# Optimization experiments

Measured on AMD Instinct MI355X. Metric: run time of the kernel, lower is better.

Reference implementation:

```python
import jax, jax.numpy as jnp
import numpy as np


def setup_inputs() -> dict:
    key = jax.random.key(0)
    k1, k2, k3, k4 = jax.random.split(key, 4)
    B, C, H, W = 4, 64, 128, 256
    Cout, kH, kW = 64, 3, 3
    x = jax.random.normal(k1, (B, C, H, W), dtype=jnp.float32)
    # offset layout: channel 2*(i*kW+j) = dy, 2*(i*kW+j)+1 = dx (deformable_groups=1)
    offset = jax.random.normal(k2, (B, 2 * kH * kW, H, W), dtype=jnp.float32)
    weight = jax.random.normal(k3, (Cout, C, kH, kW), dtype=jnp.float32) * 0.05
    bias = jax.random.normal(k4, (Cout,), dtype=jnp.float32) * 0.05
    return {"x": x, "offset": offset, "weight": weight, "bias": bias}


STRIDE, PAD, DIL = 1, 1, 1


def _deform_conv(x, offset, weight, bias):
    B, C, H, W = x.shape
    Cout, Cin, kH, kW = weight.shape
    K = kH * kW
    Ho = (H + 2 * PAD - DIL * (kH - 1) - 1) // STRIDE + 1
    Wo = (W + 2 * PAD - DIL * (kW - 1) - 1) // STRIDE + 1

    hs = (jnp.arange(Ho) * STRIDE - PAD).astype(jnp.float32)  # [Ho]
    ws = (jnp.arange(Wo) * STRIDE - PAD).astype(jnp.float32)  # [Wo]
    ki, kj = jnp.meshgrid(jnp.arange(kH), jnp.arange(kW), indexing="ij")
    ki = (ki.reshape(K) * DIL).astype(jnp.float32)  # [K]
    kj = (kj.reshape(K) * DIL).astype(jnp.float32)

    off = offset.reshape(B, K, 2, Ho, Wo)
    dy, dx = off[:, :, 0], off[:, :, 1]  # [B,K,Ho,Wo]
    py = hs[None, None, :, None] + ki[None, :, None, None] + dy  # [B,K,Ho,Wo]
    px = ws[None, None, None, :] + kj[None, :, None, None] + dx

    y0 = jnp.floor(py)
    x0 = jnp.floor(px)
    ly = py - y0
    lx = px - x0
    y0i = y0.astype(jnp.int32)
    x0i = x0.astype(jnp.int32)

    def gather(xb, yi, xi):
        # xb: [C,H,W]; yi, xi: [K,Ho,Wo]; zero for out-of-bounds corners
        valid = (yi >= 0) & (yi < H) & (xi >= 0) & (xi < W)
        yc = jnp.clip(yi, 0, H - 1)
        xc = jnp.clip(xi, 0, W - 1)
        idx = (yc * W + xc).reshape(-1)
        g = jnp.take(xb.reshape(C, H * W), idx, axis=1).reshape(C, K, Ho, Wo)
        return g * valid[None].astype(xb.dtype)

    gather_b = jax.vmap(gather)
    corners = [
        (y0i, x0i, (1.0 - ly) * (1.0 - lx)),
        (y0i, x0i + 1, (1.0 - ly) * lx),
        (y0i + 1, x0i, ly * (1.0 - lx)),
        (y0i + 1, x0i + 1, ly * lx),
    ]
    vals = jnp.zeros((B, C, K, Ho, Wo), dtype=x.dtype)
    for yi, xi, w in corners:
        vals = vals + gather_b(x, yi, xi) * w[:, None]  # broadcast over C

    out = jnp.einsum("bckhw,ock->bohw", vals, weight.reshape(Cout, Cin, K))
    return out + bias[None, :, None, None]


def reference(x, offset, weight, bias):
    return _deform_conv(x, offset, weight, bias)
```

## Files before the change

kernel.cpp:

```cpp
#include <hip/hip_runtime.h>

typedef float floatx4 __attribute__((ext_vector_type(4)));
typedef _Float16 half2v __attribute__((ext_vector_type(2)));
typedef _Float16 half8 __attribute__((ext_vector_type(8)));

#define Hh 128
#define Ww 256
#define Cc 64
#define COUT 64
#define Bb 4
#define HW (Hh*Ww)
#define VP 74

__global__ void prep(const float* __restrict__ x, const float* __restrict__ wsrc,
                     _Float16* __restrict__ xn, unsigned short* __restrict__ wdst) {
    const int bx = blockIdx.x, h = blockIdx.y, b = blockIdx.z;
    const int tid = threadIdx.x;
    if (bx == 2) {
        const int i = (h + Hh * b) * 72 + tid;
        if (tid < 72) {
            const int kt = i % 9, c = (i / 9) % Cc, o = i / (9 * Cc);
            _Float16 hv = (_Float16)wsrc[i];
            wdst[(kt * COUT + o) * Cc + c] = *(unsigned short*)&hv;
        }
        return;
    }
    __shared__ unsigned short T[128][VP];
    const int wl = tid & 127;
    const int ch = tid >> 7;
    const float* sp = x + ((b * Cc + ch * 32) * Hh + h) * Ww + bx * 128 + wl;
#pragma unroll
    for (int c2 = 0; c2 < 16; ++c2) {
        const float v0 = sp[(2 * c2) * HW];
        const float v1 = sp[(2 * c2 + 1) * HW];
        half2v hv; hv.x = (_Float16)v0; hv.y = (_Float16)v1;
        *(unsigned*)&T[wl][ch * 32 + 2 * c2] = *(unsigned*)&hv;
    }
    __syncthreads();
    uint4* drow = (uint4*)(xn + ((size_t)(b * Hh + h) * Ww + bx * 128) * 64);
#pragma unroll
    for (int j = 0; j < 4; ++j) {
        const int idx = j * 256 + tid;
        drow[idx] = *(const uint4*)&T[idx >> 3][(idx & 7) * 8];
    }
}

__device__ __forceinline__ void lds_barrier() {
    asm volatile("s_waitcnt lgkmcnt(0)\n\ts_barrier" ::: "memory");
}

struct Tap {
    half2v W00, W01, W10, W11;
    int a00, a01, a10, a11;
};

__device__ __forceinline__ void tap_setup(int kt, int h, int w, float dy, float dx,
                                          int cg, Tap& t) {
    const int ki = kt / 3, kj = kt % 3;
    const float py = (float)(h - 1 + ki) + dy;
    const float px = (float)(w - 1 + kj) + dx;
    const float y0f = floorf(py), x0f = floorf(px);
    const int y0 = (int)y0f, x0 = (int)x0f;
    const float ly = py - y0f, lx = px - x0f;
    const int y1 = y0 + 1, x1 = x0 + 1;
    const bool vy0 = ((unsigned)y0 < Hh), vy1 = ((unsigned)y1 < Hh);
    const bool vx0 = ((unsigned)x0 < Ww), vx1 = ((unsigned)x1 < Ww);
    const float w00 = (vy0 && vx0) ? (1.f - ly) * (1.f - lx) : 0.f;
    const float w01 = (vy0 && vx1) ? (1.f - ly) * lx : 0.f;
    const float w10 = (vy1 && vx0) ? ly * (1.f - lx) : 0.f;
    const float w11 = (vy1 && vx1) ? ly * lx : 0.f;
    _Float16 h00 = (_Float16)w00, h01 = (_Float16)w01;
    _Float16 h10 = (_Float16)w10, h11 = (_Float16)w11;
    t.W00.x = h00; t.W00.y = h00;  t.W01.x = h01; t.W01.y = h01;
    t.W10.x = h10; t.W10.y = h10;  t.W11.x = h11; t.W11.y = h11;
    const int y0c = min(max(y0, 0), Hh - 1), y1c = min(max(y1, 0), Hh - 1);
    const int x0c = min(max(x0, 0), Ww - 1), x1c = min(max(x1, 0), Ww - 1);
    t.a00 = (y0c * Ww + x0c) * 8 + cg;
    t.a01 = (y0c * Ww + x1c) * 8 + cg;
    t.a10 = (y1c * Ww + x0c) * 8 + cg;
    t.a11 = (y1c * Ww + x1c) * 8 + cg;
}

__device__ __forceinline__ void tap_load(const uint4* __restrict__ xb4, const Tap& t,
                                         unsigned (&pf)[16]) {
    *(uint4*)&pf[0]  = xb4[t.a00];
    *(uint4*)&pf[4]  = xb4[t.a01];
    *(uint4*)&pf[8]  = xb4[t.a10];
    *(uint4*)&pf[12] = xb4[t.a11];
}

__device__ __forceinline__ void wf_load(const unsigned short* __restrict__ wt,
                                        half8 (&WF)[4]) {
    WF[0] = *(const half8*)(wt);
    WF[1] = *(const half8*)(wt + 16 * Cc);
    WF[2] = *(const half8*)(wt + 32);
    WF[3] = *(const half8*)(wt + 16 * Cc + 32);
}

__device__ __forceinline__ void tap_store(const Tap& t, const unsigned (&pf)[16],
                                          unsigned short* __restrict__ vrow) {
    unsigned o[4];
#pragma unroll
    for (int s = 0; s < 4; ++s) {
        half2v v = (*(const half2v*)&pf[s])      * t.W00
                 + (*(const half2v*)&pf[4 + s])  * t.W01
                 + (*(const half2v*)&pf[8 + s])  * t.W10
                 + (*(const half2v*)&pf[12 + s]) * t.W11;
        o[s] = *(unsigned*)&v;
    }
    uint4 u; u.x = o[0]; u.y = o[1]; u.z = o[2]; u.w = o[3];
    *(uint4*)vrow = u;
}

__device__ __forceinline__ void mfma_tap(const half8 (&WF)[4],
                                         const unsigned short* __restrict__ Vbuf,
                                         int nt, int ln, floatx4 (&acc)[2]) {
#pragma unroll
    for (int g = 0; g < 2; ++g) {
        const int pp = nt * 16 + (ln & 15);
        half8 bfrag = *(const half8*)&Vbuf[pp * VP + g * 32 + (ln >> 4) * 8];
        acc[0] = __builtin_amdgcn_mfma_f32_16x16x32_f16(WF[2 * g],     bfrag, acc[0], 0, 0, 0);
        acc[1] = __builtin_amdgcn_mfma_f32_16x16x32_f16(WF[2 * g + 1], bfrag, acc[1], 0, 0, 0);
    }
}

template<int KT>
__device__ __forceinline__ void pipe_iter(
    const uint4* __restrict__ xb4, const float* __restrict__ offb,
    const unsigned short* __restrict__ wfb,
    const unsigned short* __restrict__ V0, const unsigned short* __restrict__ V1,
    unsigned short* __restrict__ vrow0, unsigned short* __restrict__ vrow1,
    int h, int w, int cg, int nt, int ln,
    Tap& tp0, Tap& tp1, unsigned (&pf0)[16], unsigned (&pf1)[16],
    half8 (&WF0)[4], half8 (&WF1)[4],
    float& dy0, float& dx0, float& dy1, float& dx1,
    floatx4 (&acc)[2])
{
    constexpr int S = KT & 1, T = 1 - S;
    wf_load(wfb + KT * COUT * Cc, S ? WF1 : WF0);
    if constexpr (KT < 8) {
        tap_setup(KT + 1, h, w, T ? dy1 : dy0, T ? dx1 : dx0, cg, T ? tp1 : tp0);
        tap_load(xb4, T ? tp1 : tp0, T ? pf1 : pf0);
    }
    if constexpr (KT + 3 <= 8) {
        (T ? dy1 : dy0) = offb[(2 * (KT + 3)) * HW];
        (T ? dx1 : dx0) = offb[(2 * (KT + 3) + 1) * HW];
    }
    mfma_tap(T ? WF1 : WF0, T ? V1 : V0, nt, ln, acc);
    tap_store(S ? tp1 : tp0, S ? pf1 : pf0, S ? vrow1 : vrow0);
    lds_barrier();
}

__launch_bounds__(256, 4)
__global__ void dcn_mfma(const _Float16* __restrict__ xn,
                         const float* __restrict__ offset,
                         const unsigned short* __restrict__ wb,
                         const float* __restrict__ bias,
                         float* __restrict__ out) {
    __shared__ unsigned short V[2][32 * VP];

    const int tid = threadIdx.x;
    const int p   = tid >> 3;
    const int cg  = tid & 7;
    const int wv  = tid >> 6;
    const int ln  = tid & 63;

    const int b  = blockIdx.z;
    const int h  = blockIdx.y;
    const int w0 = blockIdx.x * 32;
    const int w  = w0 + p;

    const uint4* xb4  = (const uint4*)(xn + (size_t)b * HW * 64);
    const float* offb = offset + b * 18 * HW + h * Ww + w;
    unsigned short* vrow0 = &V[0][p * VP + cg * 8];
    unsigned short* vrow1 = &V[1][p * VP + cg * 8];

    const int nt = wv & 1;
    const int mb = (wv >> 1) * 2;
    const unsigned short* wfb = wb + (mb * 16 + (ln & 15)) * Cc + (ln >> 4) * 8;

    floatx4 acc[2];
    acc[0] = (floatx4)0.f; acc[1] = (floatx4)0.f;

    unsigned pf0[16], pf1[16];
    half8 WF0[4], WF1[4];
    Tap tp0, tp1;

    float dy0 = offb[0],        dx0 = offb[HW];
    float dy1 = offb[2 * HW],   dx1 = offb[3 * HW];
    wf_load(wfb, WF0);
    tap_setup(0, h, w, dy0, dx0, cg, tp0);
    tap_load(xb4, tp0, pf0);
    tap_setup(1, h, w, dy1, dx1, cg, tp1);
    tap_load(xb4, tp1, pf1);
    dy0 = offb[4 * HW]; dx0 = offb[5 * HW];
    dy1 = offb[6 * HW]; dx1 = offb[7 * HW];
    tap_store(tp0, pf0, vrow0);
    lds_barrier();

#define PI(K) pipe_iter<K>(xb4, offb, wfb, V[0], V[1], vrow0, vrow1, h, w, cg, nt, ln, \
                           tp0, tp1, pf0, pf1, WF0, WF1, dy0, dx0, dy1, dx1, acc)
    PI(1); PI(2); PI(3); PI(4); PI(5); PI(6); PI(7); PI(8);
#undef PI

    mfma_tap(WF0, V[0], nt, ln, acc);

    float* outp = out + b * COUT * HW + h * Ww;
    const int col = w0 + nt * 16 + (ln & 15);
#pragma unroll
    for (int mi = 0; mi < 2; ++mi)
#pragma unroll
        for (int r = 0; r < 4; ++r) {
            const int o = (mb + mi) * 16 + (ln >> 4) * 4 + r;
            outp[o * HW + col] = acc[mi][r] + bias[o];
        }
}

extern "C" void kernel_launch(void* const* d_in, const int* in_sizes, int n_in,
                              void* d_out, int out_size, void* d_ws, size_t ws_size,
                              hipStream_t stream) {
    const float* x      = (const float*)d_in[0];
    const float* offset = (const float*)d_in[1];
    const float* weight = (const float*)d_in[2];
    const float* bias   = (const float*)d_in[3];
    float* out = (float*)d_out;

    _Float16* xn = (_Float16*)d_ws;
    unsigned short* wb = (unsigned short*)((char*)d_ws + (size_t)Bb * HW * Cc * 2);

    prep<<<dim3(3, Hh, Bb), 256, 0, stream>>>(x, weight, xn, wb);
    dcn_mfma<<<dim3(Ww / 32, Hh, Bb), 256, 0, stream>>>(xn, offset, wb, bias, out);
}
```

Baseline: 176.3 us.

## Build MFMA B-fragments in registers directly, dropping LDS staging and barriers

Each wave now gathers and bilinearly combines the sampled pixels straight into its own MFMA B-operand registers, so every lane covers one output column and one 8-channel group. The shared-memory V buffer and the per-tap barriers are removed. Each wave computes all 64 output channels for 16 columns (4 accumulators), and each block covers 64 columns instead of 32. In exchange, every wave has to load all weight fragments itself, and the gather loads are split into two half-channel stages per tap, which raises register pressure.

```diff
diff --git a/kernel.cpp b/kernel.cpp
--- a/kernel.cpp
+++ b/kernel.cpp
@@ -45,17 +45,13 @@
     }
 }
 
-__device__ __forceinline__ void lds_barrier() {
-    asm volatile("s_waitcnt lgkmcnt(0)\n\ts_barrier" ::: "memory");
-}
-
-struct Tap {
+struct TapS {
     half2v W00, W01, W10, W11;
     int a00, a01, a10, a11;
 };
 
 __device__ __forceinline__ void tap_setup(int kt, int h, int w, float dy, float dx,
-                                          int cg, Tap& t) {
+                                          int kg, TapS& t) {
     const int ki = kt / 3, kj = kt % 3;
     const float py = (float)(h - 1 + ki) + dy;
     const float px = (float)(w - 1 + kj) + dx;
@@ -75,80 +71,62 @@
     t.W10.x = h10; t.W10.y = h10;  t.W11.x = h11; t.W11.y = h11;
     const int y0c = min(max(y0, 0), Hh - 1), y1c = min(max(y1, 0), Hh - 1);
     const int x0c = min(max(x0, 0), Ww - 1), x1c = min(max(x1, 0), Ww - 1);
-    t.a00 = (y0c * Ww + x0c) * 8 + cg;
-    t.a01 = (y0c * Ww + x1c) * 8 + cg;
-    t.a10 = (y1c * Ww + x0c) * 8 + cg;
-    t.a11 = (y1c * Ww + x1c) * 8 + cg;
+    t.a00 = (y0c * Ww + x0c) * 8 + kg;
+    t.a01 = (y0c * Ww + x1c) * 8 + kg;
+    t.a10 = (y1c * Ww + x0c) * 8 + kg;
+    t.a11 = (y1c * Ww + x1c) * 8 + kg;
 }
 
-__device__ __forceinline__ void tap_load(const uint4* __restrict__ xb4, const Tap& t,
-                                         unsigned (&pf)[16]) {
-    *(uint4*)&pf[0]  = xb4[t.a00];
-    *(uint4*)&pf[4]  = xb4[t.a01];
-    *(uint4*)&pf[8]  = xb4[t.a10];
-    *(uint4*)&pf[12] = xb4[t.a11];
+__device__ __forceinline__ half8 combine4(const TapS& t, const uint4 (&c)[4]) {
+    union { unsigned u[4]; half8 h; } r;
+    const half2v* p0 = (const half2v*)&c[0];
+    const half2v* p1 = (const half2v*)&c[1];
+    const half2v* p2 = (const half2v*)&c[2];
+    const half2v* p3 = (const half2v*)&c[3];
+#pragma unroll
+    for (int s = 0; s < 4; ++s) {
+        half2v v = p0[s] * t.W00 + p1[s] * t.W01 + p2[s] * t.W10 + p3[s] * t.W11;
+        r.u[s] = *(unsigned*)&v;
+    }
+    return r.h;
 }
 
-__device__ __forceinline__ void wf_load(const unsigned short* __restrict__ wt,
-                                        half8 (&WF)[4]) {
-    WF[0] = *(const half8*)(wt);
-    WF[1] = *(const half8*)(wt + 16 * Cc);
-    WF[2] = *(const half8*)(wt + 32);
-    WF[3] = *(const half8*)(wt + 16 * Cc + 32);
-}
-
-__device__ __forceinline__ void tap_store(const Tap& t, const unsigned (&pf)[16],
-                                          unsigned short* __restrict__ vrow) {
-    unsigned o[4];
-#pragma unroll
-    for (int s = 0; s < 4; ++s) {
-        half2v v = (*(const half2v*)&pf[s])      * t.W00
-                 + (*(const half2v*)&pf[4 + s])  * t.W01
-                 + (*(const half2v*)&pf[8 + s])  * t.W10
-                 + (*(const half2v*)&pf[12 + s]) * t.W11;
-        o[s] = *(unsigned*)&v;
-    }
-    uint4 u; u.x = o[0]; u.y = o[1]; u.z = o[2]; u.w = o[3];
-    *(uint4*)vrow = u;
-}
-
-__device__ __forceinline__ void mfma_tap(const half8 (&WF)[4],
-                                         const unsigned short* __restrict__ Vbuf,
-                                         int nt, int ln, floatx4 (&acc)[2]) {
-#pragma unroll
-    for (int g = 0; g < 2; ++g) {
-        const int pp = nt * 16 + (ln & 15);
-        half8 bfrag = *(const half8*)&Vbuf[pp * VP + g * 32 + (ln >> 4) * 8];
-        acc[0] = __builtin_amdgcn_mfma_f32_16x16x32_f16(WF[2 * g],     bfrag, acc[0], 0, 0, 0);
-        acc[1] = __builtin_amdgcn_mfma_f32_16x16x32_f16(WF[2 * g + 1], bfrag, acc[1], 0, 0, 0);
-    }
-}
-
-template<int KT>
-__device__ __forceinline__ void pipe_iter(
+template<int S>
+__device__ __forceinline__ void stage(
     const uint4* __restrict__ xb4, const float* __restrict__ offb,
     const unsigned short* __restrict__ wfb,
-    const unsigned short* __restrict__ V0, const unsigned short* __restrict__ V1,
-    unsigned short* __restrict__ vrow0, unsigned short* __restrict__ vrow1,
-    int h, int w, int cg, int nt, int ln,
-    Tap& tp0, Tap& tp1, unsigned (&pf0)[16], unsigned (&pf1)[16],
-    half8 (&WF0)[4], half8 (&WF1)[4],
-    float& dy0, float& dx0, float& dy1, float& dx1,
-    floatx4 (&acc)[2])
+    int h, int w, int kg,
+    TapS& t0, TapS& t1, uint4 (&cb)[2][4],
+    float (&oy)[2], float (&ox)[2],
+    floatx4 (&acc)[4])
 {
-    constexpr int S = KT & 1, T = 1 - S;
-    wf_load(wfb + KT * COUT * Cc, S ? WF1 : WF0);
-    if constexpr (KT < 8) {
-        tap_setup(KT + 1, h, w, T ? dy1 : dy0, T ? dx1 : dx0, cg, T ? tp1 : tp0);
-        tap_load(xb4, T ? tp1 : tp0, T ? pf1 : pf0);
+    constexpr int KT = S >> 1, G = S & 1;
+    TapS& tS = (KT & 1) ? t1 : t0;
+
+    half8 WF[4];
+#pragma unroll
+    for (int mi = 0; mi < 4; ++mi)
+        WF[mi] = *(const half8*)(wfb + KT * COUT * Cc + mi * 16 * Cc + G * 32);
+
+    if constexpr (G == 0) {
+        if constexpr (KT + 2 <= 8) {
+            oy[KT & 1] = offb[(2 * (KT + 2)) * HW];
+            ox[KT & 1] = offb[(2 * (KT + 2) + 1) * HW];
+        }
+        cb[1][0] = xb4[tS.a00 + 4]; cb[1][1] = xb4[tS.a01 + 4];
+        cb[1][2] = xb4[tS.a10 + 4]; cb[1][3] = xb4[tS.a11 + 4];
+    } else if constexpr (KT < 8) {
+        TapS& tT = (KT & 1) ? t0 : t1;
+        tap_setup(KT + 1, h, w, oy[(KT + 1) & 1], ox[(KT + 1) & 1], kg, tT);
+        cb[0][0] = xb4[tT.a00]; cb[0][1] = xb4[tT.a01];
+        cb[0][2] = xb4[tT.a10]; cb[0][3] = xb4[tT.a11];
     }
-    if constexpr (KT + 3 <= 8) {
-        (T ? dy1 : dy0) = offb[(2 * (KT + 3)) * HW];
-        (T ? dx1 : dx0) = offb[(2 * (KT + 3) + 1) * HW];
-    }
-    mfma_tap(T ? WF1 : WF0, T ? V1 : V0, nt, ln, acc);
-    tap_store(S ? tp1 : tp0, S ? pf1 : pf0, S ? vrow1 : vrow0);
-    lds_barrier();
+
+    half8 bf = combine4(tS, cb[G]);
+
+#pragma unroll
+    for (int mi = 0; mi < 4; ++mi)
+        acc[mi] = __builtin_amdgcn_mfma_f32_16x16x32_f16(WF[mi], bf, acc[mi], 0, 0, 0);
 }
 
 __launch_bounds__(256, 4)
@@ -157,62 +135,47 @@
                          const unsigned short* __restrict__ wb,
                          const float* __restrict__ bias,
                          float* __restrict__ out) {
-    __shared__ unsigned short V[2][32 * VP];
-
     const int tid = threadIdx.x;
-    const int p   = tid >> 3;
-    const int cg  = tid & 7;
+    const int ln  = tid & 63;
     const int wv  = tid >> 6;
-    const int ln  = tid & 63;
-
-    const int b  = blockIdx.z;
-    const int h  = blockIdx.y;
-    const int w0 = blockIdx.x * 32;
-    const int w  = w0 + p;
+    const int b   = blockIdx.z;
+    const int h   = blockIdx.y;
+    const int w0  = blockIdx.x * 64 + wv * 16;
+    const int pos = ln & 15;
+    const int kg  = ln >> 4;
+    const int w   = w0 + pos;
 
     const uint4* xb4  = (const uint4*)(xn + (size_t)b * HW * 64);
     const float* offb = offset + b * 18 * HW + h * Ww + w;
-    unsigned short* vrow0 = &V[0][p * VP + cg * 8];
-    unsigned short* vrow1 = &V[1][p * VP + cg * 8];
+    const unsigned short* wfb = wb + pos * Cc + kg * 8;
 
-    const int nt = wv & 1;
-    const int mb = (wv >> 1) * 2;
-    const unsigned short* wfb = wb + (mb * 16 + (ln & 15)) * Cc + (ln >> 4) * 8;
+    floatx4 acc[4];
+#pragma unroll
+    for (int mi = 0; mi < 4; ++mi) acc[mi] = (floatx4)0.f;
 
-    floatx4 acc[2];
-    acc[0] = (floatx4)0.f; acc[1] = (floatx4)0.f;
+    uint4 cb[2][4];
+    TapS t0, t1;
+    float oy[2], ox[2];
 
-    unsigned pf0[16], pf1[16];
-    half8 WF0[4], WF1[4];
-    Tap tp0, tp1;
+    oy[0] = offb[0];        ox[0] = offb[HW];
+    oy[1] = offb[2 * HW];   ox[1] = offb[3 * HW];
+    tap_setup(0, h, w, oy[0], ox[0], kg, t0);
+    cb[0][0] = xb4[t0.a00]; cb[0][1] = xb4[t0.a01];
+    cb[0][2] = xb4[t0.a10]; cb[0][3] = xb4[t0.a11];
 
-    float dy0 = offb[0],        dx0 = offb[HW];
-    float dy1 = offb[2 * HW],   dx1 = offb[3 * HW];
-    wf_load(wfb, WF0);
-    tap_setup(0, h, w, dy0, dx0, cg, tp0);
-    tap_load(xb4, tp0, pf0);
-    tap_setup(1, h, w, dy1, dx1, cg, tp1);
-    tap_load(xb4, tp1, pf1);
-    dy0 = offb[4 * HW]; dx0 = offb[5 * HW];
-    dy1 = offb[6 * HW]; dx1 = offb[7 * HW];
-    tap_store(tp0, pf0, vrow0);
-    lds_barrier();
+#define ST(S) stage<S>(xb4, offb, wfb, h, w, kg, t0, t1, cb, oy, ox, acc)
+    ST(0);  ST(1);  ST(2);  ST(3);  ST(4);  ST(5);
+    ST(6);  ST(7);  ST(8);  ST(9);  ST(10); ST(11);
+    ST(12); ST(13); ST(14); ST(15); ST(16); ST(17);
+#undef ST
 
-#define PI(K) pipe_iter<K>(xb4, offb, wfb, V[0], V[1], vrow0, vrow1, h, w, cg, nt, ln, \
-                           tp0, tp1, pf0, pf1, WF0, WF1, dy0, dx0, dy1, dx1, acc)
-    PI(1); PI(2); PI(3); PI(4); PI(5); PI(6); PI(7); PI(8);
-#undef PI
-
-    mfma_tap(WF0, V[0], nt, ln, acc);
-
-    float* outp = out + b * COUT * HW + h * Ww;
-    const int col = w0 + nt * 16 + (ln & 15);
+    float* outp = out + b * COUT * HW + h * Ww + w0 + pos;
 #pragma unroll
-    for (int mi = 0; mi < 2; ++mi)
+    for (int mi = 0; mi < 4; ++mi)
 #pragma unroll
         for (int r = 0; r < 4; ++r) {
-            const int o = (mb + mi) * 16 + (ln >> 4) * 4 + r;
-            outp[o * HW + col] = acc[mi][r] + bias[o];
+            const int o = mi * 16 + kg * 4 + r;
+            outp[o * HW] = acc[mi][r] + bias[o];
         }
 }
 
@@ -229,5 +192,5 @@
     unsigned short* wb = (unsigned short*)((char*)d_ws + (size_t)Bb * HW * Cc * 2);
 
     prep<<<dim3(3, Hh, Bb), 256, 0, stream>>>(x, weight, xn, wb);
-    dcn_mfma<<<dim3(Ww / 32, Hh, Bb), 256, 0, stream>>>(xn, offset, wb, bias, out);
+    dcn_mfma<<<dim3(Ww / 64, Hh, Bb), 256, 0, stream>>>(xn, offset, wb, bias, out);
 }
```

Result: slower. 217.8 us (+23.5%).
